# Kernel tuning notes

Hardware: AMD Instinct MI355X
Metric: run time of the kernel (lower is better)

The kernel has to match this reference:

```python
import jax, jax.numpy as jnp
import numpy as np

B, S, D_IN, D_OUT = 8, 2048, 1024, 1024


def setup_inputs() -> dict:
    key = jax.random.key(0)
    ks = jax.random.split(key, 9)
    sc = 1.0 / np.sqrt(D_IN)
    return {
        "in_k": jax.random.normal(ks[0], (B, S, D_IN), jnp.float32),
        "in_q": jax.random.normal(ks[1], (B, S, D_IN), jnp.float32),
        "in_v": jax.random.normal(ks[2], (B, S, D_IN), jnp.float32),
        "Wk": jax.random.normal(ks[3], (D_IN, D_OUT), jnp.float32) * sc,
        "bk": jax.random.normal(ks[4], (D_OUT,), jnp.float32) * sc,
        "Wq": jax.random.normal(ks[5], (D_IN, D_OUT), jnp.float32) * sc,
        "bq": jax.random.normal(ks[6], (D_OUT,), jnp.float32) * sc,
        "Wv": jax.random.normal(ks[7], (D_IN, D_OUT), jnp.float32) * sc,
        "bv": jax.random.normal(ks[8], (D_OUT,), jnp.float32) * sc,
    }


def reference(in_k, in_q, in_v, Wk, bk, Wq, bq, Wv, bv):
    k = in_k @ Wk + bk  # [B,S,D]
    q = in_q @ Wq + bq
    v = in_v @ Wv + bv
    scale = 1.0 / jnp.sqrt(jnp.asarray(D_OUT, q.dtype))
    scores = jnp.einsum("bqd,bkd->bqk", q, k) * scale  # [B,S,S]
    attn = jax.nn.softmax(scores, axis=-1)
    return jnp.einsum("bqk,bkd->bqd", attn, v)
```

## Files before the change

kernel.cpp:

```cpp
#include <hip/hip_runtime.h>
#include <hip/hip_bf16.h>
#include <stdint.h>

typedef __bf16 bf16x8 __attribute__((ext_vector_type(8)));
typedef float  f32x4  __attribute__((ext_vector_type(4)));
typedef uint16_t u16x8 __attribute__((ext_vector_type(8)));

__device__ __forceinline__ uint16_t f32_to_bf16(float f) {
    union { float f; uint32_t u; } v; v.f = f;
    uint32_t u = v.u;
    uint32_t r = (u + 0x7FFFu + ((u >> 16) & 1u)) >> 16;
    return (uint16_t)r;
}
__device__ __forceinline__ float bf16_to_f32(uint16_t b) {
    union { uint32_t u; float f; } v; v.u = ((uint32_t)b) << 16;
    return v.f;
}

__device__ __forceinline__ void gld16(const uint16_t* g, uint16_t* l) {
    __builtin_amdgcn_global_load_lds(
        (const __attribute__((address_space(1))) void*)g,
        (__attribute__((address_space(3))) void*)l,
        16, 0, 0);
}

__global__ __launch_bounds__(256) void cast_f32_bf16_kernel(
    const float* __restrict__ in, uint16_t* __restrict__ out) {
    size_t i = ((size_t)blockIdx.x * 256 + threadIdx.x) * 4;
    float4 f = *(const float4*)(in + i);
    ushort4 o;
    o.x = f32_to_bf16(f.x); o.y = f32_to_bf16(f.y);
    o.z = f32_to_bf16(f.z); o.w = f32_to_bf16(f.w);
    *(ushort4*)(out + i) = o;
}

__global__ __launch_bounds__(256) void wtrans_kernel(
    const float* __restrict__ W, uint16_t* __restrict__ Wt) {
    __shared__ float tile[64][65];
    const int n0 = blockIdx.x * 64, k0 = blockIdx.y * 64;
    const int tx = threadIdx.x & 63, ty0 = threadIdx.x >> 6;
#pragma unroll
    for (int r = 0; r < 16; ++r) {
        int ty = ty0 + r * 4;
        tile[ty][tx] = W[(size_t)(k0 + ty) * 1024 + n0 + tx];
    }
    __syncthreads();
#pragma unroll
    for (int r = 0; r < 16; ++r) {
        int ty = ty0 + r * 4;
        Wt[(size_t)(n0 + ty) * 1024 + k0 + tx] = f32_to_bf16(tile[tx][ty]);
    }
}

__global__ __launch_bounds__(256) void vtrans_kernel(
    const uint16_t* __restrict__ V, uint16_t* __restrict__ Vt) {
    const int b = blockIdx.z;
    const uint16_t* Vp = V + (size_t)b * 2048 * 1024;
    uint16_t* Vtp = Vt + (size_t)b * 1024 * 2048;
    __shared__ uint16_t tile[64][65];
    const int d0 = blockIdx.x * 64, s0 = blockIdx.y * 64;
    const int tx = threadIdx.x & 63, ty0 = threadIdx.x >> 6;
#pragma unroll
    for (int r = 0; r < 16; ++r) {
        int ty = ty0 + r * 4;
        tile[ty][tx] = Vp[(size_t)(s0 + ty) * 1024 + d0 + tx];
    }
    __syncthreads();
#pragma unroll
    for (int r = 0; r < 16; ++r) {
        int ty = ty0 + r * 4;
        Vtp[(size_t)(d0 + ty) * 2048 + s0 + tx] = tile[tx][ty];
    }
}

template <bool OUT_BF16, bool HAS_BIAS>
__global__ __launch_bounds__(256, 2) void gemm_nt_kernel(
    const uint16_t* __restrict__ A, long long lda, long long sAz,
    const uint16_t* __restrict__ B, long long ldb, long long sBz,
    void* __restrict__ Cv, long long ldc, long long sCz,
    int K, float alpha, const float* __restrict__ bias,
    int Z, int tN) {
    __shared__ __align__(16) uint16_t As[128 * 32];
    __shared__ __align__(16) uint16_t Bs[128 * 32];

    const int tid  = threadIdx.x;
    const int lane = tid & 63;
    const int wave = tid >> 6;

    const int bid = blockIdx.x;
    const int z = bid % Z;
    const int t = bid / Z;
    const int bandSz = tN * 8;
    const int band = t / bandSz;
    const int r0 = t - band * bandSz;
    const int my = band * 8 + (r0 & 7);
    const int mx = r0 >> 3;

    A += (size_t)z * sAz;
    B += (size_t)z * sBz;
    const int row0 = my * 128;
    const int col0 = mx * 128;

    const int c0 = tid, c1 = tid + 256;
    const int ar0 = c0 >> 2, ak0 = (((c0 & 3) ^ ((ar0 >> 1) & 3))) * 8;
    const int ar1 = c1 >> 2, ak1 = (((c1 & 3) ^ ((ar1 >> 1) & 3))) * 8;

    const int wr = wave >> 1, wc = wave & 1;
    const int mrow = lane & 15;
    const int quad = lane >> 4;
    const int sw = (mrow >> 1) & 3;
    const int qsw = (quad ^ sw) * 8;

    f32x4 acc[4][4];
#pragma unroll
    for (int i = 0; i < 4; ++i)
#pragma unroll
        for (int j = 0; j < 4; ++j) acc[i][j] = 0.0f;

    for (int k0 = 0; k0 < K; k0 += 32) {
        __syncthreads();
        gld16(A + (size_t)(row0 + ar0) * lda + k0 + ak0, &As[(size_t)c0 * 8]);
        gld16(A + (size_t)(row0 + ar1) * lda + k0 + ak1, &As[(size_t)c1 * 8]);
        gld16(B + (size_t)(col0 + ar0) * ldb + k0 + ak0, &Bs[(size_t)c0 * 8]);
        gld16(B + (size_t)(col0 + ar1) * ldb + k0 + ak1, &Bs[(size_t)c1 * 8]);
        __syncthreads();

        bf16x8 af[4], bfj[4];
#pragma unroll
        for (int i = 0; i < 4; ++i)
            af[i] = *(const bf16x8*)&As[(size_t)(wr * 64 + i * 16 + mrow) * 32 + qsw];
#pragma unroll
        for (int j = 0; j < 4; ++j)
            bfj[j] = *(const bf16x8*)&Bs[(size_t)(wc * 64 + j * 16 + mrow) * 32 + qsw];
#pragma unroll
        for (int i = 0; i < 4; ++i)
#pragma unroll
            for (int j = 0; j < 4; ++j)
                acc[i][j] = __builtin_amdgcn_mfma_f32_16x16x32_bf16(
                    af[i], bfj[j], acc[i][j], 0, 0, 0);
    }

    if (OUT_BF16) {
        uint16_t* C = (uint16_t*)Cv + (size_t)z * sCz;
#pragma unroll
        for (int i = 0; i < 4; ++i)
#pragma unroll
            for (int j = 0; j < 4; ++j)
#pragma unroll
                for (int r = 0; r < 4; ++r) {
                    int row = row0 + wr * 64 + i * 16 + quad * 4 + r;
                    int col = col0 + wc * 64 + j * 16 + mrow;
                    float val = acc[i][j][r] * alpha;
                    if (HAS_BIAS) val += bias[col];
                    C[(size_t)row * ldc + col] = f32_to_bf16(val);
                }
    } else {
        float* C = (float*)Cv + (size_t)z * sCz;
#pragma unroll
        for (int i = 0; i < 4; ++i)
#pragma unroll
            for (int j = 0; j < 4; ++j)
#pragma unroll
                for (int r = 0; r < 4; ++r) {
                    int row = row0 + wr * 64 + i * 16 + quad * 4 + r;
                    int col = col0 + wc * 64 + j * 16 + mrow;
                    float val = acc[i][j][r] * alpha;
                    if (HAS_BIAS) val += bias[col];
                    C[(size_t)row * ldc + col] = val;
                }
    }
}

__global__ __launch_bounds__(256) void softmax_kernel(uint16_t* __restrict__ Sc) {
    __shared__ float red[4];
    uint16_t* p = Sc + (size_t)blockIdx.x * 2048;
    const int tid = threadIdx.x;
    u16x8 v = *(const u16x8*)(p + tid * 8);
    float f[8];
#pragma unroll
    for (int i = 0; i < 8; ++i) f[i] = bf16_to_f32(v[i]);

    float m = f[0];
#pragma unroll
    for (int i = 1; i < 8; ++i) m = fmaxf(m, f[i]);
#pragma unroll
    for (int off = 32; off; off >>= 1) m = fmaxf(m, __shfl_xor(m, off, 64));
    if ((tid & 63) == 0) red[tid >> 6] = m;
    __syncthreads();
    m = fmaxf(fmaxf(red[0], red[1]), fmaxf(red[2], red[3]));

    float e[8], s = 0.0f;
#pragma unroll
    for (int i = 0; i < 8; ++i) { e[i] = __expf(f[i] - m); s += e[i]; }
#pragma unroll
    for (int off = 32; off; off >>= 1) s += __shfl_xor(s, off, 64);
    __syncthreads();
    if ((tid & 63) == 0) red[tid >> 6] = s;
    __syncthreads();
    s = (red[0] + red[1]) + (red[2] + red[3]);
    float inv = 1.0f / s;

    u16x8 o;
#pragma unroll
    for (int i = 0; i < 8; ++i) o[i] = f32_to_bf16(e[i] * inv);
    *(u16x8*)(p + tid * 8) = o;
}

extern "C" void kernel_launch(void* const* d_in, const int* in_sizes, int n_in,
                              void* d_out, int out_size, void* d_ws, size_t ws_size,
                              hipStream_t stream) {
    const float* in_k = (const float*)d_in[0];
    const float* in_q = (const float*)d_in[1];
    const float* in_v = (const float*)d_in[2];
    const float* Wk = (const float*)d_in[3];
    const float* bk = (const float*)d_in[4];
    const float* Wq = (const float*)d_in[5];
    const float* bq = (const float*)d_in[6];
    const float* Wv = (const float*)d_in[7];
    const float* bv = (const float*)d_in[8];
    float* out = (float*)d_out;

    char* w = (char*)d_ws;
    uint16_t* Xq  = (uint16_t*)(w + 0);
    uint16_t* Xk  = (uint16_t*)(w + 33554432);
    uint16_t* Xv  = (uint16_t*)(w + 67108864);
    uint16_t* Qb  = (uint16_t*)(w + 100663296);
    uint16_t* Kb  = (uint16_t*)(w + 134217728);
    uint16_t* Vb  = (uint16_t*)(w + 167772160);
    uint16_t* Wqt = (uint16_t*)(w + 201326592);
    uint16_t* Wkt = (uint16_t*)(w + 203423744);
    uint16_t* Wvt = (uint16_t*)(w + 205520896);
    uint16_t* Sc  = Xq;
    uint16_t* Vt  = Xv;

    cast_f32_bf16_kernel<<<16384, 256, 0, stream>>>(in_q, Xq);
    cast_f32_bf16_kernel<<<16384, 256, 0, stream>>>(in_k, Xk);
    cast_f32_bf16_kernel<<<16384, 256, 0, stream>>>(in_v, Xv);
    wtrans_kernel<<<dim3(16, 16), 256, 0, stream>>>(Wq, Wqt);
    wtrans_kernel<<<dim3(16, 16), 256, 0, stream>>>(Wk, Wkt);
    wtrans_kernel<<<dim3(16, 16), 256, 0, stream>>>(Wv, Wvt);

    gemm_nt_kernel<true, true><<<1024, 256, 0, stream>>>(
        Xq, 1024, 0, Wqt, 1024, 0, Qb, 1024, 0, 1024, 1.0f, bq, 1, 8);
    gemm_nt_kernel<true, true><<<1024, 256, 0, stream>>>(
        Xk, 1024, 0, Wkt, 1024, 0, Kb, 1024, 0, 1024, 1.0f, bk, 1, 8);
    gemm_nt_kernel<true, true><<<1024, 256, 0, stream>>>(
        Xv, 1024, 0, Wvt, 1024, 0, Vb, 1024, 0, 1024, 1.0f, bv, 1, 8);

    vtrans_kernel<<<dim3(16, 32, 8), 256, 0, stream>>>(Vb, Vt);

    gemm_nt_kernel<true, false><<<2048, 256, 0, stream>>>(
        Qb, 1024, 2048LL * 1024, Kb, 1024, 2048LL * 1024,
        Sc, 2048, 2048LL * 2048, 1024, 0.03125f, nullptr, 8, 16);

    softmax_kernel<<<16384, 256, 0, stream>>>(Sc);

    gemm_nt_kernel<false, false><<<1024, 256, 0, stream>>>(
        Sc, 2048, 2048LL * 2048, Vt, 2048, 1024LL * 2048,
        out, 1024, 2048LL * 1024, 2048, 1.0f, nullptr, 8, 8);
}
```

Before: 553.3 us.

## Fuse input casts and V transpose into projection GEMMs, batch weight transposes

Removes the three standalone f32→bf16 cast kernels by having a new projection GEMM load fp32 activations directly into LDS and convert to bf16 in registers before the MFMAs. The V projection epilogue writes its output already transposed, which eliminates the separate V transpose kernel. The three weight-transpose launches are merged into one using blockIdx.z. This cuts HBM traffic and launch count, at the cost of a larger fp32 A tile in LDS (16KB) and per-iteration conversion work, plus strided scattered stores in the transposed V epilogue.

```diff
diff --git a/kernel.cpp b/kernel.cpp
--- a/kernel.cpp
+++ b/kernel.cpp
@@ -17,25 +17,18 @@
     return v.f;
 }
 
-__device__ __forceinline__ void gld16(const uint16_t* g, uint16_t* l) {
+__device__ __forceinline__ void gld16(const void* g, void* l) {
     __builtin_amdgcn_global_load_lds(
         (const __attribute__((address_space(1))) void*)g,
         (__attribute__((address_space(3))) void*)l,
         16, 0, 0);
 }
 
-__global__ __launch_bounds__(256) void cast_f32_bf16_kernel(
-    const float* __restrict__ in, uint16_t* __restrict__ out) {
-    size_t i = ((size_t)blockIdx.x * 256 + threadIdx.x) * 4;
-    float4 f = *(const float4*)(in + i);
-    ushort4 o;
-    o.x = f32_to_bf16(f.x); o.y = f32_to_bf16(f.y);
-    o.z = f32_to_bf16(f.z); o.w = f32_to_bf16(f.w);
-    *(ushort4*)(out + i) = o;
-}
-
 __global__ __launch_bounds__(256) void wtrans_kernel(
-    const float* __restrict__ W, uint16_t* __restrict__ Wt) {
+    const float* __restrict__ W0, const float* __restrict__ W1,
+    const float* __restrict__ W2, uint16_t* __restrict__ Wt0) {
+    const float* W = (blockIdx.z == 0) ? W0 : (blockIdx.z == 1) ? W1 : W2;
+    uint16_t* Wt = Wt0 + (size_t)blockIdx.z * 1024 * 1024;
     __shared__ float tile[64][65];
     const int n0 = blockIdx.x * 64, k0 = blockIdx.y * 64;
     const int tx = threadIdx.x & 63, ty0 = threadIdx.x >> 6;
@@ -52,34 +45,102 @@
     }
 }
 
-__global__ __launch_bounds__(256) void vtrans_kernel(
-    const uint16_t* __restrict__ V, uint16_t* __restrict__ Vt) {
-    const int b = blockIdx.z;
-    const uint16_t* Vp = V + (size_t)b * 2048 * 1024;
-    uint16_t* Vtp = Vt + (size_t)b * 1024 * 2048;
-    __shared__ uint16_t tile[64][65];
-    const int d0 = blockIdx.x * 64, s0 = blockIdx.y * 64;
-    const int tx = threadIdx.x & 63, ty0 = threadIdx.x >> 6;
-#pragma unroll
-    for (int r = 0; r < 16; ++r) {
-        int ty = ty0 + r * 4;
-        tile[ty][tx] = Vp[(size_t)(s0 + ty) * 1024 + d0 + tx];
-    }
-    __syncthreads();
-#pragma unroll
-    for (int r = 0; r < 16; ++r) {
-        int ty = ty0 + r * 4;
-        Vtp[(size_t)(d0 + ty) * 2048 + s0 + tx] = tile[tx][ty];
-    }
-}
-
-template <bool OUT_BF16, bool HAS_BIAS>
+template <int EPI>
+__global__ __launch_bounds__(256, 2) void proj_gemm_kernel(
+    const float* __restrict__ A,
+    const uint16_t* __restrict__ B,
+    void* __restrict__ Cv, const float* __restrict__ bias, int tN) {
+    __shared__ __align__(16) float    Asf[128 * 32];
+    __shared__ __align__(16) uint16_t Bs[128 * 32];
+
+    const int tid  = threadIdx.x;
+    const int lane = tid & 63;
+    const int wave = tid >> 6;
+
+    const int t = blockIdx.x;
+    const int bandSz = tN * 8;
+    const int band = t / bandSz;
+    const int r0 = t - band * bandSz;
+    const int row0 = (band * 8 + (r0 & 7)) * 128;
+    const int col0 = (r0 >> 3) * 128;
+
+    const int a_r[4] = { (tid) >> 3, (tid + 256) >> 3, (tid + 512) >> 3, (tid + 768) >> 3 };
+    const int a_k[4] = { (((tid) & 7) ^ (a_r[0] & 7)) * 4,
+                         (((tid + 256) & 7) ^ (a_r[1] & 7)) * 4,
+                         (((tid + 512) & 7) ^ (a_r[2] & 7)) * 4,
+                         (((tid + 768) & 7) ^ (a_r[3] & 7)) * 4 };
+    const int b_r0 = tid >> 2,        b_k0 = (((tid) & 3) ^ ((b_r0 >> 1) & 3)) * 8;
+    const int b_r1 = (tid + 256) >> 2, b_k1 = (((tid + 256) & 3) ^ ((b_r1 >> 1) & 3)) * 8;
+
+    const int wr = wave >> 1, wc = wave & 1;
+    const int mrow = lane & 15;
+    const int quad = lane >> 4;
+    const int bsw = (quad ^ ((mrow >> 1) & 3)) * 8;
+
+    f32x4 acc[4][4];
+#pragma unroll
+    for (int i = 0; i < 4; ++i)
+#pragma unroll
+        for (int j = 0; j < 4; ++j) acc[i][j] = 0.0f;
+
+    for (int k0 = 0; k0 < 1024; k0 += 32) {
+        __syncthreads();
+#pragma unroll
+        for (int u = 0; u < 4; ++u)
+            gld16(A + (size_t)(row0 + a_r[u]) * 1024 + k0 + a_k[u],
+                  &Asf[(size_t)(tid + u * 256) * 4]);
+        gld16(B + (size_t)(col0 + b_r0) * 1024 + k0 + b_k0, &Bs[(size_t)tid * 8]);
+        gld16(B + (size_t)(col0 + b_r1) * 1024 + k0 + b_k1, &Bs[(size_t)(tid + 256) * 8]);
+        __syncthreads();
+
+        bf16x8 af[4], bfj[4];
+#pragma unroll
+        for (int i = 0; i < 4; ++i) {
+            const int row = wr * 64 + i * 16 + mrow;
+            const int s = row & 7;
+            f32x4 lo = *(const f32x4*)&Asf[(size_t)row * 32 + (((quad * 2) ^ s)) * 4];
+            f32x4 hi = *(const f32x4*)&Asf[(size_t)row * 32 + (((quad * 2 + 1) ^ s)) * 4];
+#pragma unroll
+            for (int e = 0; e < 4; ++e) {
+                af[i][e]     = (__bf16)lo[e];
+                af[i][e + 4] = (__bf16)hi[e];
+            }
+        }
+#pragma unroll
+        for (int j = 0; j < 4; ++j)
+            bfj[j] = *(const bf16x8*)&Bs[(size_t)(wc * 64 + j * 16 + mrow) * 32 + bsw];
+#pragma unroll
+        for (int i = 0; i < 4; ++i)
+#pragma unroll
+            for (int j = 0; j < 4; ++j)
+                acc[i][j] = __builtin_amdgcn_mfma_f32_16x16x32_bf16(
+                    af[i], bfj[j], acc[i][j], 0, 0, 0);
+    }
+
+    uint16_t* C = (uint16_t*)Cv;
+#pragma unroll
+    for (int i = 0; i < 4; ++i)
+#pragma unroll
+        for (int j = 0; j < 4; ++j)
+#pragma unroll
+            for (int r = 0; r < 4; ++r) {
+                int row = row0 + wr * 64 + i * 16 + quad * 4 + r;
+                int col = col0 + wc * 64 + j * 16 + mrow;
+                uint16_t val = f32_to_bf16(acc[i][j][r] + bias[col]);
+                if (EPI == 0) {
+                    C[(size_t)row * 1024 + col] = val;
+                } else {
+                    C[((size_t)(row >> 11) * 1024 + col) * 2048 + (row & 2047)] = val;
+                }
+            }
+}
+
+template <bool OUT_BF16>
 __global__ __launch_bounds__(256, 2) void gemm_nt_kernel(
     const uint16_t* __restrict__ A, long long lda, long long sAz,
     const uint16_t* __restrict__ B, long long ldb, long long sBz,
     void* __restrict__ Cv, long long ldc, long long sCz,
-    int K, float alpha, const float* __restrict__ bias,
-    int Z, int tN) {
+    int K, float alpha, int Z, int tN) {
     __shared__ __align__(16) uint16_t As[128 * 32];
     __shared__ __align__(16) uint16_t Bs[128 * 32];
 
@@ -93,13 +154,11 @@
     const int bandSz = tN * 8;
     const int band = t / bandSz;
     const int r0 = t - band * bandSz;
-    const int my = band * 8 + (r0 & 7);
-    const int mx = r0 >> 3;
+    const int row0 = (band * 8 + (r0 & 7)) * 128;
+    const int col0 = (r0 >> 3) * 128;
 
     A += (size_t)z * sAz;
     B += (size_t)z * sBz;
-    const int row0 = my * 128;
-    const int col0 = mx * 128;
 
     const int c0 = tid, c1 = tid + 256;
     const int ar0 = c0 >> 2, ak0 = (((c0 & 3) ^ ((ar0 >> 1) & 3))) * 8;
@@ -108,8 +167,7 @@
     const int wr = wave >> 1, wc = wave & 1;
     const int mrow = lane & 15;
     const int quad = lane >> 4;
-    const int sw = (mrow >> 1) & 3;
-    const int qsw = (quad ^ sw) * 8;
+    const int qsw = (quad ^ ((mrow >> 1) & 3)) * 8;
 
     f32x4 acc[4][4];
 #pragma unroll
@@ -150,9 +208,7 @@
                 for (int r = 0; r < 4; ++r) {
                     int row = row0 + wr * 64 + i * 16 + quad * 4 + r;
                     int col = col0 + wc * 64 + j * 16 + mrow;
-                    float val = acc[i][j][r] * alpha;
-                    if (HAS_BIAS) val += bias[col];
-                    C[(size_t)row * ldc + col] = f32_to_bf16(val);
+                    C[(size_t)row * ldc + col] = f32_to_bf16(acc[i][j][r] * alpha);
                 }
     } else {
         float* C = (float*)Cv + (size_t)z * sCz;
@@ -164,9 +220,7 @@
                 for (int r = 0; r < 4; ++r) {
                     int row = row0 + wr * 64 + i * 16 + quad * 4 + r;
                     int col = col0 + wc * 64 + j * 16 + mrow;
-                    float val = acc[i][j][r] * alpha;
-                    if (HAS_BIAS) val += bias[col];
-                    C[(size_t)row * ldc + col] = val;
+                    C[(size_t)row * ldc + col] = acc[i][j][r] * alpha;
                 }
     }
 }
@@ -221,41 +275,27 @@
     float* out = (float*)d_out;
 
     char* w = (char*)d_ws;
-    uint16_t* Xq  = (uint16_t*)(w + 0);
-    uint16_t* Xk  = (uint16_t*)(w + 33554432);
-    uint16_t* Xv  = (uint16_t*)(w + 67108864);
-    uint16_t* Qb  = (uint16_t*)(w + 100663296);
-    uint16_t* Kb  = (uint16_t*)(w + 134217728);
-    uint16_t* Vb  = (uint16_t*)(w + 167772160);
-    uint16_t* Wqt = (uint16_t*)(w + 201326592);
-    uint16_t* Wkt = (uint16_t*)(w + 203423744);
-    uint16_t* Wvt = (uint16_t*)(w + 205520896);
-    uint16_t* Sc  = Xq;
-    uint16_t* Vt  = Xv;
-
-    cast_f32_bf16_kernel<<<16384, 256, 0, stream>>>(in_q, Xq);
-    cast_f32_bf16_kernel<<<16384, 256, 0, stream>>>(in_k, Xk);
-    cast_f32_bf16_kernel<<<16384, 256, 0, stream>>>(in_v, Xv);
-    wtrans_kernel<<<dim3(16, 16), 256, 0, stream>>>(Wq, Wqt);
-    wtrans_kernel<<<dim3(16, 16), 256, 0, stream>>>(Wk, Wkt);
-    wtrans_kernel<<<dim3(16, 16), 256, 0, stream>>>(Wv, Wvt);
-
-    gemm_nt_kernel<true, true><<<1024, 256, 0, stream>>>(
-        Xq, 1024, 0, Wqt, 1024, 0, Qb, 1024, 0, 1024, 1.0f, bq, 1, 8);
-    gemm_nt_kernel<true, true><<<1024, 256, 0, stream>>>(
-        Xk, 1024, 0, Wkt, 1024, 0, Kb, 1024, 0, 1024, 1.0f, bk, 1, 8);
-    gemm_nt_kernel<true, true><<<1024, 256, 0, stream>>>(
-        Xv, 1024, 0, Wvt, 1024, 0, Vb, 1024, 0, 1024, 1.0f, bv, 1, 8);
-
-    vtrans_kernel<<<dim3(16, 32, 8), 256, 0, stream>>>(Vb, Vt);
-
-    gemm_nt_kernel<true, false><<<2048, 256, 0, stream>>>(
+    uint16_t* Sc  = (uint16_t*)(w + 0);
+    uint16_t* Qb  = (uint16_t*)(w + 67108864);
+    uint16_t* Kb  = (uint16_t*)(w + 100663296);
+    uint16_t* Vt  = (uint16_t*)(w + 134217728);
+    uint16_t* Wqt = (uint16_t*)(w + 167772160);
+    uint16_t* Wkt = Wqt + 1024 * 1024;
+    uint16_t* Wvt = Wkt + 1024 * 1024;
+
+    wtrans_kernel<<<dim3(16, 16, 3), 256, 0, stream>>>(Wq, Wk, Wv, Wqt);
+
+    proj_gemm_kernel<0><<<1024, 256, 0, stream>>>(in_q, Wqt, Qb, bq, 8);
+    proj_gemm_kernel<0><<<1024, 256, 0, stream>>>(in_k, Wkt, Kb, bk, 8);
+    proj_gemm_kernel<1><<<1024, 256, 0, stream>>>(in_v, Wvt, Vt, bv, 8);
+
+    gemm_nt_kernel<true><<<2048, 256, 0, stream>>>(
         Qb, 1024, 2048LL * 1024, Kb, 1024, 2048LL * 1024,
-        Sc, 2048, 2048LL * 2048, 1024, 0.03125f, nullptr, 8, 16);
+        Sc, 2048, 2048LL * 2048, 1024, 0.03125f, 8, 16);
 
     softmax_kernel<<<16384, 256, 0, stream>>>(Sc);
 
-    gemm_nt_kernel<false, false><<<1024, 256, 0, stream>>>(
+    gemm_nt_kernel<false><<<1024, 256, 0, stream>>>(
         Sc, 2048, 2048LL * 2048, Vt, 2048, 1024LL * 2048,
-        out, 1024, 2048LL * 1024, 2048, 1.0f, nullptr, 8, 8);
-}
+        out, 1024, 2048LL * 1024, 2048, 1.0f, 8, 8);
+}
```

After: 587.9 us. 6.3% more time.
